# Performance work log

Measured on AMD Instinct MI355X. Metric: run time of the kernel, lower is better.

Reference implementation:

```python
import jax, jax.numpy as jnp
import numpy as np

N = 100000      # n_nodes
E = 1600000     # n_edges (avg degree 16)
F_IN = 128      # nfeat
H = 128         # nhid
C = 64          # nclass


def setup_inputs() -> dict:
    key = jax.random.key(0)
    ks = jax.random.split(key, 6)
    x = jax.random.normal(ks[0], (N, F_IN), dtype=jnp.float32)
    edge_index = jax.random.randint(ks[1], (2, E), 0, N, dtype=jnp.int32)
    # Glorot-ish init for GCNConv weights, zeros for bias (PyG default)
    W1 = jax.random.normal(ks[2], (F_IN, H), dtype=jnp.float32) * (1.0 / np.sqrt(F_IN))
    b1 = jnp.zeros((H,), dtype=jnp.float32)
    W2 = jax.random.normal(ks[3], (H, C), dtype=jnp.float32) * (1.0 / np.sqrt(H))
    b2 = jnp.zeros((C,), dtype=jnp.float32)
    return {"x": x, "edge_index": edge_index, "W1": W1, "b1": b1, "W2": W2, "b2": b2}


def _gcn_conv(x, W, b, src, dst, n):
    """PyG GCNConv: h = W^T x, out_i = sum_j norm_ij * h_j + b, with
    symmetric normalization over the self-loop-augmented graph."""
    h = x @ W                                                   # [n, out]
    deg = jax.ops.segment_sum(jnp.ones(src.shape[0], h.dtype), dst, num_segments=n)
    dinv = jnp.where(deg > 0, jax.lax.rsqrt(deg), 0.0)          # D^-1/2
    norm = dinv[src] * dinv[dst]                                # [E+n]
    msg = h[src] * norm[:, None]                                # gather + scale
    out = jax.ops.segment_sum(msg, dst, num_segments=n)         # scatter-add
    return out + b


def reference(x, edge_index, W1, b1, W2, b2):
    loop = jnp.arange(N, dtype=edge_index.dtype)
    src = jnp.concatenate([edge_index[0], loop])  # sources j (with self loops)
    dst = jnp.concatenate([edge_index[1], loop])  # targets i
    h = jax.nn.relu(_gcn_conv(x, W1, b1, src, dst, N))  # dropout = identity (eval)
    out = _gcn_conv(h, W2, b2, src, dst, N)
    return jax.nn.log_softmax(out, axis=1)
```

## Files before the change

### kernel.cpp

```cpp
#include <hip/hip_runtime.h>
#include <hip/hip_fp16.h>
#include <cstdint>
#include <cstddef>
#include <cstring>


__device__ inline unsigned pack_bf16x2(float a, float b) {
    unsigned ua = __float_as_uint(a);
    unsigned ub = __float_as_uint(b);
    ua += 0x7fffu + ((ua >> 16) & 1u);
    ub += 0x7fffu + ((ub >> 16) & 1u);
    return (ua >> 16) | (ub & 0xffff0000u);
}
__device__ inline unsigned short bf16_rne(float v) {
    unsigned u = __float_as_uint(v);
    u += 0x7fffu + ((u >> 16) & 1u);
    return (unsigned short)(u >> 16);
}
__device__ inline float bf16lo(unsigned u) { return __uint_as_float(u << 16); }
__device__ inline float bf16hi(unsigned u) { return __uint_as_float(u & 0xffff0000u); }


typedef float fv2 __attribute__((ext_vector_type(2)));

template <bool HI>
__device__ inline float2 fp8x2_to_f32_sel(unsigned u) {
#if __has_builtin(__builtin_amdgcn_cvt_pk_f32_fp8)
    fv2 r = __builtin_amdgcn_cvt_pk_f32_fp8((int)u, HI);
    return make_float2(r.x, r.y);
#else
    unsigned u2 = HI ? (u >> 16) : (u & 0xffffu);
    unsigned w = (u2 & 0xFFu) | ((u2 & 0xFF00u) << 8);
    unsigned hb = ((w & 0x00800080u) << 8) | ((w & 0x007f007fu) << 7);
    __half2 h2;
    memcpy(&h2, &hb, 4);
    float2 f = __half22float2(h2);
    f.x *= 256.0f;
    f.y *= 256.0f;
    return f;
#endif
}

__device__ inline unsigned f32_to_fp8_byte(float v) {
    unsigned short hb = __half_as_ushort(__float2half(v * 0.00390625f));
    unsigned t = hb & 0x7fffu;
    t += 0x3fu + ((t >> 7) & 1u);
    return ((hb >> 8) & 0x80u) | (t >> 7);
}

__device__ inline unsigned char f32_to_fp8_b(float v) {
#if __has_builtin(__builtin_amdgcn_cvt_pk_fp8_f32)
    return (unsigned char)(__builtin_amdgcn_cvt_pk_fp8_f32(v, v, 0, false) & 0xff);
#else
    return (unsigned char)f32_to_fp8_byte(v);
#endif
}

typedef int iv4 __attribute__((ext_vector_type(4)));

#define NPART 8
#define KB    32
#define NPP_MAX 12500


__global__ void k_zero16(int* __restrict__ p) {
    if (threadIdx.x < 16) p[threadIdx.x] = 0;
}

__global__ __launch_bounds__(256) void k_bcount(const int* __restrict__ dst,
                                                int* __restrict__ bucketCount,
                                                int E, int npp) {
    __shared__ int c8[NPART];
    if (threadIdx.x < NPART) c8[threadIdx.x] = 0;
    __syncthreads();
    int t = blockIdx.x * blockDim.x + threadIdx.x;
    int stride = gridDim.x * blockDim.x;
    int E4 = E >> 2;
    const iv4* d4 = (const iv4*)dst;
    for (int i = t; i < E4; i += stride) {
        iv4 d = d4[i];
        atomicAdd(&c8[(unsigned)d.x / (unsigned)npp], 1);
        atomicAdd(&c8[(unsigned)d.y / (unsigned)npp], 1);
        atomicAdd(&c8[(unsigned)d.z / (unsigned)npp], 1);
        atomicAdd(&c8[(unsigned)d.w / (unsigned)npp], 1);
    }
    for (int e = E4 * 4 + t; e < E; e += stride)
        atomicAdd(&c8[(unsigned)dst[e] / (unsigned)npp], 1);
    __syncthreads();
    if (threadIdx.x < NPART) atomicAdd(&bucketCount[threadIdx.x], c8[threadIdx.x]);
}

__global__ void k_bscan(const int* __restrict__ bucketCount,
                        int* __restrict__ bucketBase,
                        int* __restrict__ bucketCursor) {
    if (threadIdx.x == 0) {
        int run = 0;
        for (int p = 0; p < NPART; ++p) {
            bucketBase[p] = run;
            bucketCursor[p] = run;
            run += bucketCount[p];
        }
    }
}

__global__ __launch_bounds__(256) void k_bucket(const int* __restrict__ src,
                                                const int* __restrict__ dst,
                                                int* __restrict__ bucketCursor,
                                                int2* __restrict__ pairs,
                                                int E, int npp) {
    __shared__ int cnt8[NPART], run8[NPART], gbase8[NPART];
    int tid = threadIdx.x;
    int base_e = blockIdx.x * 4096 + tid * 16;
    int nv = min(16, E - base_e);
    if (nv < 0) nv = 0;
    int dv[16], sv[16];
    if (nv == 16) {
        for (int q = 0; q < 4; ++q) {
            iv4 d = *(const iv4*)(dst + base_e + q * 4);
            iv4 s = *(const iv4*)(src + base_e + q * 4);
            dv[q * 4 + 0] = d.x; dv[q * 4 + 1] = d.y; dv[q * 4 + 2] = d.z; dv[q * 4 + 3] = d.w;
            sv[q * 4 + 0] = s.x; sv[q * 4 + 1] = s.y; sv[q * 4 + 2] = s.z; sv[q * 4 + 3] = s.w;
        }
    } else {
        for (int k = 0; k < nv; ++k) { dv[k] = dst[base_e + k]; sv[k] = src[base_e + k]; }
    }
    if (tid < NPART) { cnt8[tid] = 0; run8[tid] = 0; }
    __syncthreads();
    for (int k = 0; k < nv; ++k)
        atomicAdd(&cnt8[(unsigned)dv[k] / (unsigned)npp], 1);
    __syncthreads();
    if (tid < NPART) gbase8[tid] = atomicAdd(&bucketCursor[tid], cnt8[tid]);
    __syncthreads();
    for (int k = 0; k < nv; ++k) {
        int p = (unsigned)dv[k] / (unsigned)npp;
        int r = atomicAdd(&run8[p], 1);
        int2 pr; pr.x = dv[k]; pr.y = sv[k];
        pairs[gbase8[p] + r] = pr;
    }
}

__global__ __launch_bounds__(256) void k_count_part(const int2* __restrict__ pairs,
                                                    const int* __restrict__ bucketBase,
                                                    const int* __restrict__ bucketCount,
                                                    int* __restrict__ cntarr, int npp) {
    __shared__ int h[NPP_MAX];
    int p = blockIdx.x & (NPART - 1);
    int b = blockIdx.x >> 3;
    int lo = p * npp;
    for (int i = threadIdx.x; i < npp; i += 256) h[i] = 0;
    __syncthreads();
    int segBase = bucketBase[p], sz = bucketCount[p];
    int chunk = (sz + KB - 1) / KB;
    int s0 = segBase + b * chunk;
    int s1 = min(segBase + sz, s0 + chunk);
    for (int i = s0 + threadIdx.x; i < s1; i += 256)
        atomicAdd(&h[pairs[i].x - lo], 1);
    __syncthreads();
    size_t out = (size_t)(p * KB + b) * npp;
    for (int i = threadIdx.x; i < npp; i += 256) cntarr[out + i] = h[i];
}

__global__ void k_indeg(const int* __restrict__ cntarr, int* __restrict__ indeg,
                        int n, int npp) {
    int d = blockIdx.x * blockDim.x + threadIdx.x;
    if (d >= n) return;
    int p = (unsigned)d / (unsigned)npp;
    int dl = d - p * npp;
    size_t base = (size_t)p * KB * npp + dl;
    int s = 0;
    for (int b = 0; b < KB; ++b) s += cntarr[base + (size_t)b * npp];
    indeg[d] = s;
}

__global__ void k_scan_local(const int* __restrict__ in, int* __restrict__ out,
                             int* __restrict__ partials, int n) {
    __shared__ int s[256];
    int t = threadIdx.x;
    int base = blockIdx.x * 1024 + t * 4;
    int v0 = (base + 0) < n ? in[base + 0] : 0;
    int v1 = (base + 1) < n ? in[base + 1] : 0;
    int v2 = (base + 2) < n ? in[base + 2] : 0;
    int v3 = (base + 3) < n ? in[base + 3] : 0;
    int sum = v0 + v1 + v2 + v3;
    s[t] = sum;
    __syncthreads();
    for (int off = 1; off < 256; off <<= 1) {
        int x = (t >= off) ? s[t - off] : 0;
        __syncthreads();
        s[t] += x;
        __syncthreads();
    }
    int excl = s[t] - sum;
    if ((base + 0) < n) out[base + 0] = excl;
    if ((base + 1) < n) out[base + 1] = excl + v0;
    if ((base + 2) < n) out[base + 2] = excl + v0 + v1;
    if ((base + 3) < n) out[base + 3] = excl + v0 + v1 + v2;
    if (t == 255) partials[blockIdx.x] = s[255];
}

__global__ void k_scan_partials(int* __restrict__ partials, int np) {
    __shared__ int s[256];
    int t = threadIdx.x;
    int v = (t < np) ? partials[t] : 0;
    s[t] = v;
    __syncthreads();
    for (int off = 1; off < 256; off <<= 1) {
        int x = (t >= off) ? s[t - off] : 0;
        __syncthreads();
        s[t] += x;
        __syncthreads();
    }
    if (t < np) partials[t] = s[t] - v;
}

__global__ void k_finalize(int* __restrict__ row_ptr, const int* __restrict__ partials,
                           const int* __restrict__ indeg, float* __restrict__ dinv,
                           int n, int E) {
    int i = blockIdx.x * blockDim.x + threadIdx.x;
    if (i < n) {
        int rp = row_ptr[i] + partials[i >> 10];
        row_ptr[i] = rp;
        dinv[i] = rsqrtf((float)indeg[i] + 1.0f);
        if (i == 0) row_ptr[n] = E;
    }
}

__global__ void k_bases(int* __restrict__ cntarr, const int* __restrict__ row_ptr,
                        int n, int npp) {
    int d = blockIdx.x * blockDim.x + threadIdx.x;
    if (d >= n) return;
    int p = (unsigned)d / (unsigned)npp;
    int dl = d - p * npp;
    size_t base = (size_t)p * KB * npp + dl;
    int run = row_ptr[d];
    for (int b = 0; b < KB; ++b) {
        size_t idx = base + (size_t)b * npp;
        int c = cntarr[idx];
        cntarr[idx] = run;
        run += c;
    }
}

__global__ __launch_bounds__(256) void k_fill2(const int2* __restrict__ pairs,
                                               const int* __restrict__ bucketBase,
                                               const int* __restrict__ bucketCount,
                                               const int* __restrict__ cntarr,
                                               int* __restrict__ col, int npp) {
    __shared__ int cur[NPP_MAX];
    int p = blockIdx.x & (NPART - 1);
    int b = blockIdx.x >> 3;
    int lo = p * npp;
    size_t slice = (size_t)(p * KB + b) * npp;
    for (int i = threadIdx.x; i < npp; i += 256) cur[i] = cntarr[slice + i];
    __syncthreads();
    int segBase = bucketBase[p], sz = bucketCount[p];
    int chunk = (sz + KB - 1) / KB;
    int s0 = segBase + b * chunk;
    int s1 = min(segBase + sz, s0 + chunk);
    for (int i = s0 + threadIdx.x; i < s1; i += 256) {
        int2 e = pairs[i];
        int pos = atomicAdd(&cur[e.x - lo], 1);
        col[pos] = e.y;
    }
}

typedef __attribute__((ext_vector_type(8))) short short8;
typedef __attribute__((ext_vector_type(4))) float f32x4;

union FragU {
    short8 s;
    uint4 u4;
    unsigned u[4];
};

template <int NOUT>
__global__ void k_packW(const float* __restrict__ W, unsigned* __restrict__ Bp) {
    const int NT = NOUT / 16;
    int nf = 4 * NT * 64;
    for (int fid = threadIdx.x; fid < nf; fid += 256) {
        int q = fid / (NT * 64);
        int rem = fid - q * NT * 64;
        int nt = rem >> 6;
        int lane = rem & 63;
        int k0 = q * 32 + (lane >> 4) * 8;
        int ncol = nt * 16 + (lane & 15);
        unsigned u[4];
        for (int h = 0; h < 4; ++h) {
            float a = W[(k0 + 2 * h) * NOUT + ncol];
            float b = W[(k0 + 2 * h + 1) * NOUT + ncol];
            u[h] = pack_bf16x2(a, b);
        }
        uint4 o = {u[0], u[1], u[2], u[3]};
        *(uint4*)(Bp + (size_t)fid * 4) = o;
    }
}

__global__ __launch_bounds__(256) void k_gemm128_mfma(const float* __restrict__ X,
                                                      const unsigned* __restrict__ Bp,
                                                      const float* __restrict__ dinv,
                                                      unsigned char* __restrict__ H8,
                                                      int n) {
    int w = threadIdx.x >> 6;
    int lane = threadIdx.x & 63;
    int quad = lane >> 4;
    int lrow = lane & 15;
    int row0 = blockIdx.x * 64 + w * 16;
    int rowA = min(row0 + lrow, n - 1);

    f32x4 acc[8];
    for (int nt = 0; nt < 8; ++nt) acc[nt] = (f32x4){0.f, 0.f, 0.f, 0.f};

    for (int q = 0; q < 4; ++q) {
        const float* xp = X + (size_t)rowA * 128 + q * 32 + quad * 8;
        float4 x0 = *(const float4*)xp;
        float4 x1 = *(const float4*)(xp + 4);
        FragU a;
        a.u[0] = pack_bf16x2(x0.x, x0.y);
        a.u[1] = pack_bf16x2(x0.z, x0.w);
        a.u[2] = pack_bf16x2(x1.x, x1.y);
        a.u[3] = pack_bf16x2(x1.z, x1.w);
        for (int nt = 0; nt < 8; ++nt) {
            FragU b;
            b.u4 = *(const uint4*)(Bp + ((size_t)(q * 8 + nt) * 64 + lane) * 4);
            acc[nt] = __builtin_amdgcn_mfma_f32_16x16x32_bf16(a.s, b.s, acc[nt], 0, 0, 0);
        }
    }

    int rbase = row0 + quad * 4;
    float dv[4];
    if (rbase + 3 < n) {
        float4 d4 = *(const float4*)(dinv + rbase);
        dv[0] = d4.x; dv[1] = d4.y; dv[2] = d4.z; dv[3] = d4.w;
    } else {
        for (int r = 0; r < 4; ++r) dv[r] = dinv[min(rbase + r, n - 1)];
    }
    for (int nt = 0; nt < 8; ++nt) {
        for (int r = 0; r < 4; ++r) {
            int row = rbase + r;
            if (row < n)
                H8[(size_t)row * 128 + nt * 16 + lrow] = f32_to_fp8_b(dv[r] * acc[nt][r]);
        }
    }
}

__global__ __launch_bounds__(256) void k_gemm64_mfma(const unsigned* __restrict__ Xb,
                                                     const unsigned* __restrict__ Bp,
                                                     const float* __restrict__ dinv,
                                                     unsigned short* __restrict__ H16,
                                                     int n) {
    int w = threadIdx.x >> 6;
    int lane = threadIdx.x & 63;
    int quad = lane >> 4;
    int lrow = lane & 15;
    int row0 = blockIdx.x * 64 + w * 16;
    int rowA = min(row0 + lrow, n - 1);

    f32x4 acc[4];
    for (int nt = 0; nt < 4; ++nt) acc[nt] = (f32x4){0.f, 0.f, 0.f, 0.f};

    for (int q = 0; q < 4; ++q) {
        FragU a;
        a.u4 = *(const uint4*)(Xb + (size_t)rowA * 64 + q * 16 + quad * 4);
        for (int nt = 0; nt < 4; ++nt) {
            FragU b;
            b.u4 = *(const uint4*)(Bp + ((size_t)(q * 4 + nt) * 64 + lane) * 4);
            acc[nt] = __builtin_amdgcn_mfma_f32_16x16x32_bf16(a.s, b.s, acc[nt], 0, 0, 0);
        }
    }

    int rbase = row0 + quad * 4;
    float dv[4];
    if (rbase + 3 < n) {
        float4 d4 = *(const float4*)(dinv + rbase);
        dv[0] = d4.x; dv[1] = d4.y; dv[2] = d4.z; dv[3] = d4.w;
    } else {
        for (int r = 0; r < 4; ++r) dv[r] = dinv[min(rbase + r, n - 1)];
    }
    for (int nt = 0; nt < 4; ++nt) {
        for (int r = 0; r < 4; ++r) {
            int row = rbase + r;
            if (row < n)
                H16[(size_t)row * 64 + nt * 16 + lrow] = bf16_rne(dv[r] * acc[nt][r]);
        }
    }
}


__global__ __launch_bounds__(256) void k_agg_relu(const unsigned* __restrict__ hs,
                                                  const float* __restrict__ dinv,
                                                  const int* __restrict__ row_ptr,
                                                  const int* __restrict__ col,
                                                  const float* __restrict__ bias,
                                                  unsigned* __restrict__ out, int n) {
    int node = blockIdx.x * 4 + (threadIdx.x >> 6);
    if (node >= n) return;
    int lane = threadIdx.x & 63;
    int half = lane >> 5;
    int l = lane & 31;
    float a0 = 0.f, a1 = 0.f, a2 = 0.f, a3 = 0.f;
    if (half == 0) {
        unsigned u = hs[(size_t)node * 32 + l];
        float2 f01 = fp8x2_to_f32_sel<false>(u);
        float2 f23 = fp8x2_to_f32_sel<true>(u);
        a0 = f01.x; a1 = f01.y; a2 = f23.x; a3 = f23.y;
    }
    int p0 = row_ptr[node], p1 = row_ptr[node + 1];
    for (int base = p0; base < p1; base += 64) {
        int nb = min(64, p1 - base);
        int myc = col[base + min(lane, nb - 1)];
        int k = 0;
        for (; k + 16 <= nb; k += 16) {
            int jA = __shfl(myc, k + half);
            int jB = __shfl(myc, k + 2 + half);
            int jC = __shfl(myc, k + 4 + half);
            int jD = __shfl(myc, k + 6 + half);
            int jE = __shfl(myc, k + 8 + half);
            int jF = __shfl(myc, k + 10 + half);
            int jG = __shfl(myc, k + 12 + half);
            int jH = __shfl(myc, k + 14 + half);
            unsigned uA = hs[(size_t)jA * 32 + l];
            unsigned uB = hs[(size_t)jB * 32 + l];
            unsigned uC = hs[(size_t)jC * 32 + l];
            unsigned uD = hs[(size_t)jD * 32 + l];
            unsigned uE = hs[(size_t)jE * 32 + l];
            unsigned uF = hs[(size_t)jF * 32 + l];
            unsigned uG = hs[(size_t)jG * 32 + l];
            unsigned uH = hs[(size_t)jH * 32 + l];
            float2 f;
            f = fp8x2_to_f32_sel<false>(uA); a0 += f.x; a1 += f.y;
            f = fp8x2_to_f32_sel<true>(uA);  a2 += f.x; a3 += f.y;
            f = fp8x2_to_f32_sel<false>(uB); a0 += f.x; a1 += f.y;
            f = fp8x2_to_f32_sel<true>(uB);  a2 += f.x; a3 += f.y;
            f = fp8x2_to_f32_sel<false>(uC); a0 += f.x; a1 += f.y;
            f = fp8x2_to_f32_sel<true>(uC);  a2 += f.x; a3 += f.y;
            f = fp8x2_to_f32_sel<false>(uD); a0 += f.x; a1 += f.y;
            f = fp8x2_to_f32_sel<true>(uD);  a2 += f.x; a3 += f.y;
            f = fp8x2_to_f32_sel<false>(uE); a0 += f.x; a1 += f.y;
            f = fp8x2_to_f32_sel<true>(uE);  a2 += f.x; a3 += f.y;
            f = fp8x2_to_f32_sel<false>(uF); a0 += f.x; a1 += f.y;
            f = fp8x2_to_f32_sel<true>(uF);  a2 += f.x; a3 += f.y;
            f = fp8x2_to_f32_sel<false>(uG); a0 += f.x; a1 += f.y;
            f = fp8x2_to_f32_sel<true>(uG);  a2 += f.x; a3 += f.y;
            f = fp8x2_to_f32_sel<false>(uH); a0 += f.x; a1 += f.y;
            f = fp8x2_to_f32_sel<true>(uH);  a2 += f.x; a3 += f.y;
        }
        for (; k + 8 <= nb; k += 8) {
            int jA = __shfl(myc, k + half);
            int jB = __shfl(myc, k + 2 + half);
            int jC = __shfl(myc, k + 4 + half);
            int jD = __shfl(myc, k + 6 + half);
            unsigned uA = hs[(size_t)jA * 32 + l];
            unsigned uB = hs[(size_t)jB * 32 + l];
            unsigned uC = hs[(size_t)jC * 32 + l];
            unsigned uD = hs[(size_t)jD * 32 + l];
            float2 f;
            f = fp8x2_to_f32_sel<false>(uA); a0 += f.x; a1 += f.y;
            f = fp8x2_to_f32_sel<true>(uA);  a2 += f.x; a3 += f.y;
            f = fp8x2_to_f32_sel<false>(uB); a0 += f.x; a1 += f.y;
            f = fp8x2_to_f32_sel<true>(uB);  a2 += f.x; a3 += f.y;
            f = fp8x2_to_f32_sel<false>(uC); a0 += f.x; a1 += f.y;
            f = fp8x2_to_f32_sel<true>(uC);  a2 += f.x; a3 += f.y;
            f = fp8x2_to_f32_sel<false>(uD); a0 += f.x; a1 += f.y;
            f = fp8x2_to_f32_sel<true>(uD);  a2 += f.x; a3 += f.y;
        }
        for (; k < nb; k += 2) {
            int kk = k + half;
            if (kk < nb) {
                int j = __shfl(myc, kk);
                unsigned u = hs[(size_t)j * 32 + l];
                float2 f0 = fp8x2_to_f32_sel<false>(u);
                float2 f1 = fp8x2_to_f32_sel<true>(u);
                a0 += f0.x; a1 += f0.y; a2 += f1.x; a3 += f1.y;
            }
        }
    }
    a0 += __shfl_xor(a0, 32);
    a1 += __shfl_xor(a1, 32);
    a2 += __shfl_xor(a2, 32);
    a3 += __shfl_xor(a3, 32);
    float di = dinv[node];
    if (half == 0) {
        float4 b4 = *(const float4*)(bias + 4 * l);
        a0 = fmaf(di, a0, b4.x);
        a1 = fmaf(di, a1, b4.y);
        a2 = fmaf(di, a2, b4.z);
        a3 = fmaf(di, a3, b4.w);
        a0 = a0 > 0.f ? a0 : 0.f;
        a1 = a1 > 0.f ? a1 : 0.f;
        a2 = a2 > 0.f ? a2 : 0.f;
        a3 = a3 > 0.f ? a3 : 0.f;
        uint2 o = {pack_bf16x2(a0, a1), pack_bf16x2(a2, a3)};
        *(uint2*)(out + (size_t)node * 64 + 2 * l) = o;
    }
}

__global__ __launch_bounds__(256) void k_agg_lsm(const unsigned* __restrict__ hs,
                                                 const float* __restrict__ dinv,
                                                 const int* __restrict__ row_ptr,
                                                 const int* __restrict__ col,
                                                 const float* __restrict__ bias,
                                                 float* __restrict__ out, int n) {
    int node = blockIdx.x * 4 + (threadIdx.x >> 6);
    if (node >= n) return;
    int lane = threadIdx.x & 63;
    int half = lane >> 5;
    int l = lane & 31;
    float ax = 0.f, ay = 0.f;
    if (half == 0) {
        unsigned u = hs[(size_t)node * 32 + l];
        ax = bf16lo(u);
        ay = bf16hi(u);
    }
    int p0 = row_ptr[node], p1 = row_ptr[node + 1];
    for (int base = p0; base < p1; base += 64) {
        int nb = min(64, p1 - base);
        int myc = col[base + min(lane, nb - 1)];
        int k = 0;
        for (; k + 16 <= nb; k += 16) {
            int jA = __shfl(myc, k + half);
            int jB = __shfl(myc, k + 2 + half);
            int jC = __shfl(myc, k + 4 + half);
            int jD = __shfl(myc, k + 6 + half);
            int jE = __shfl(myc, k + 8 + half);
            int jF = __shfl(myc, k + 10 + half);
            int jG = __shfl(myc, k + 12 + half);
            int jH = __shfl(myc, k + 14 + half);
            unsigned uA = hs[(size_t)jA * 32 + l];
            unsigned uB = hs[(size_t)jB * 32 + l];
            unsigned uC = hs[(size_t)jC * 32 + l];
            unsigned uD = hs[(size_t)jD * 32 + l];
            unsigned uE = hs[(size_t)jE * 32 + l];
            unsigned uF = hs[(size_t)jF * 32 + l];
            unsigned uG = hs[(size_t)jG * 32 + l];
            unsigned uH = hs[(size_t)jH * 32 + l];
            ax += (bf16lo(uA) + bf16lo(uB)) + (bf16lo(uC) + bf16lo(uD)) +
                  (bf16lo(uE) + bf16lo(uF)) + (bf16lo(uG) + bf16lo(uH));
            ay += (bf16hi(uA) + bf16hi(uB)) + (bf16hi(uC) + bf16hi(uD)) +
                  (bf16hi(uE) + bf16hi(uF)) + (bf16hi(uG) + bf16hi(uH));
        }
        for (; k + 8 <= nb; k += 8) {
            int jA = __shfl(myc, k + half);
            int jB = __shfl(myc, k + 2 + half);
            int jC = __shfl(myc, k + 4 + half);
            int jD = __shfl(myc, k + 6 + half);
            unsigned uA = hs[(size_t)jA * 32 + l];
            unsigned uB = hs[(size_t)jB * 32 + l];
            unsigned uC = hs[(size_t)jC * 32 + l];
            unsigned uD = hs[(size_t)jD * 32 + l];
            ax += (bf16lo(uA) + bf16lo(uB)) + (bf16lo(uC) + bf16lo(uD));
            ay += (bf16hi(uA) + bf16hi(uB)) + (bf16hi(uC) + bf16hi(uD));
        }
        for (; k < nb; k += 2) {
            int kk = k + half;
            if (kk < nb) {
                int j = __shfl(myc, kk);
                unsigned u = hs[(size_t)j * 32 + l];
                ax += bf16lo(u);
                ay += bf16hi(u);
            }
        }
    }
    ax += __shfl_xor(ax, 32);
    ay += __shfl_xor(ay, 32);
    float di = dinv[node];
    float2 b2 = ((const float2*)bias)[l];
    float vx = fmaf(di, ax, b2.x);
    float vy = fmaf(di, ay, b2.y);
    float m = fmaxf(vx, vy);
    for (int off = 16; off; off >>= 1) m = fmaxf(m, __shfl_xor(m, off));
    float s = __expf(vx - m) + __expf(vy - m);
    for (int off = 16; off; off >>= 1) s += __shfl_xor(s, off);
    float ls = __logf(s);
    if (half == 0) {
        float2 o = {vx - m - ls, vy - m - ls};
        ((float2*)(out + (size_t)node * 64))[l] = o;
    }
}


extern "C" void kernel_launch(void* const* d_in, const int* in_sizes, int n_in,
                              void* d_out, int out_size, void* d_ws, size_t ws_size,
                              hipStream_t stream) {
    const float* x  = (const float*)d_in[0];
    const int*   ei = (const int*)d_in[1];
    const float* W1 = (const float*)d_in[2];
    const float* b1 = (const float*)d_in[3];
    const float* W2 = (const float*)d_in[4];
    const float* b2 = (const float*)d_in[5];
    float* out = (float*)d_out;

    const int N = in_sizes[0] / 128;
    const int E = in_sizes[1] / 2;
    const int* src = ei;
    const int* dst = ei + E;
    const int npp = (N + NPART - 1) / NPART;

    char* w = (char*)d_ws;
    size_t off = 0;
    auto alloc = [&](size_t bytes) -> void* {
        void* p = w + off;
        off += (bytes + 255) & ~(size_t)255;
        return p;
    };
    int*      indeg    = (int*)alloc((size_t)N * 4);
    int*      row_ptr  = (int*)alloc((size_t)(N + 1) * 4);
    int*      colarr   = (int*)alloc((size_t)E * 4);
    int*      partials = (int*)alloc(256 * 4);
    int*      bmeta    = (int*)alloc(16 * 4);
    int*      bbase    = (int*)alloc(NPART * 4);
    float*    dinv     = (float*)alloc((size_t)N * 4);
    unsigned* h1f8     = (unsigned*)alloc((size_t)N * 32 * 4);
    unsigned* a1b      = (unsigned*)alloc((size_t)N * 64 * 4);
    unsigned* h2b      = (unsigned*)alloc((size_t)N * 32 * 4);
    unsigned* Bp1      = (unsigned*)alloc(4 * 8 * 64 * 16);
    unsigned* Bp2      = (unsigned*)alloc(4 * 4 * 64 * 16);
    int2* pairs  = (int2*)a1b;
    int*  cntarr = (int*)((char*)a1b + (size_t)E * 8);
    (void)ws_size; (void)n_in; (void)out_size;

    int* bucketCount  = bmeta;
    int* bucketCursor = bmeta + 8;
    int nscan = (N + 1023) / 1024;
    int nA3 = (E + 4095) / 4096;
    int ngemm = (N + 63) / 64;

    k_zero16<<<1, 64, 0, stream>>>(bmeta);
    k_packW<128><<<1, 256, 0, stream>>>(W1, Bp1);
    k_packW<64><<<1, 256, 0, stream>>>(W2, Bp2);
    k_bcount<<<256, 256, 0, stream>>>(dst, bucketCount, E, npp);
    k_bscan<<<1, 64, 0, stream>>>(bucketCount, bbase, bucketCursor);
    k_bucket<<<nA3, 256, 0, stream>>>(src, dst, bucketCursor, pairs, E, npp);
    k_count_part<<<NPART * KB, 256, 0, stream>>>(pairs, bbase, bucketCount, cntarr, npp);
    k_indeg<<<(N + 255) / 256, 256, 0, stream>>>(cntarr, indeg, N, npp);
    k_scan_local<<<nscan, 256, 0, stream>>>(indeg, row_ptr, partials, N);
    k_scan_partials<<<1, 256, 0, stream>>>(partials, nscan);
    k_finalize<<<(N + 255) / 256, 256, 0, stream>>>(row_ptr, partials, indeg, dinv, N, E);
    k_bases<<<(N + 255) / 256, 256, 0, stream>>>(cntarr, row_ptr, N, npp);
    k_fill2<<<NPART * KB, 256, 0, stream>>>(pairs, bbase, bucketCount, cntarr,
                                            colarr, npp);

    k_gemm128_mfma<<<ngemm, 256, 0, stream>>>(x, Bp1, dinv, (unsigned char*)h1f8, N);
    k_agg_relu<<<(N + 3) / 4, 256, 0, stream>>>(h1f8, dinv, row_ptr, colarr, b1, a1b, N);
    k_gemm64_mfma<<<ngemm, 256, 0, stream>>>(a1b, Bp2, dinv, (unsigned short*)h2b, N);
    k_agg_lsm<<<(N + 3) / 4, 256, 0, stream>>>(h2b, dinv, row_ptr, colarr, b2, out, N);
}
```

Measured before the change: 302.3 us.

## Pack edge pairs into 32-bit words and fuse CSR build kernels

Edge (dst,src) pairs are packed into one 32-bit word, with the partition-local dst in the high bits and the 17-bit src in the low bits, halving bucket traffic. The zero and pack-weight kernels merge into one setup kernel. In-degree is accumulated with atomics inside the count kernel, so the separate indeg pass is gone, and finalize is fused with the per-bucket base computation. This cuts launches and memory passes in CSR construction, but the packing relies on node ids fitting in 17 bits and the local dst in 15 bits.

```diff
diff --git a/kernel.cpp b/kernel.cpp
--- a/kernel.cpp
+++ b/kernel.cpp
@@ -61,208 +61,8 @@
 #define NPART 8
 #define KB    32
 #define NPP_MAX 12500
-
-
-__global__ void k_zero16(int* __restrict__ p) {
-    if (threadIdx.x < 16) p[threadIdx.x] = 0;
-}
-
-__global__ __launch_bounds__(256) void k_bcount(const int* __restrict__ dst,
-                                                int* __restrict__ bucketCount,
-                                                int E, int npp) {
-    __shared__ int c8[NPART];
-    if (threadIdx.x < NPART) c8[threadIdx.x] = 0;
-    __syncthreads();
-    int t = blockIdx.x * blockDim.x + threadIdx.x;
-    int stride = gridDim.x * blockDim.x;
-    int E4 = E >> 2;
-    const iv4* d4 = (const iv4*)dst;
-    for (int i = t; i < E4; i += stride) {
-        iv4 d = d4[i];
-        atomicAdd(&c8[(unsigned)d.x / (unsigned)npp], 1);
-        atomicAdd(&c8[(unsigned)d.y / (unsigned)npp], 1);
-        atomicAdd(&c8[(unsigned)d.z / (unsigned)npp], 1);
-        atomicAdd(&c8[(unsigned)d.w / (unsigned)npp], 1);
-    }
-    for (int e = E4 * 4 + t; e < E; e += stride)
-        atomicAdd(&c8[(unsigned)dst[e] / (unsigned)npp], 1);
-    __syncthreads();
-    if (threadIdx.x < NPART) atomicAdd(&bucketCount[threadIdx.x], c8[threadIdx.x]);
-}
-
-__global__ void k_bscan(const int* __restrict__ bucketCount,
-                        int* __restrict__ bucketBase,
-                        int* __restrict__ bucketCursor) {
-    if (threadIdx.x == 0) {
-        int run = 0;
-        for (int p = 0; p < NPART; ++p) {
-            bucketBase[p] = run;
-            bucketCursor[p] = run;
-            run += bucketCount[p];
-        }
-    }
-}
-
-__global__ __launch_bounds__(256) void k_bucket(const int* __restrict__ src,
-                                                const int* __restrict__ dst,
-                                                int* __restrict__ bucketCursor,
-                                                int2* __restrict__ pairs,
-                                                int E, int npp) {
-    __shared__ int cnt8[NPART], run8[NPART], gbase8[NPART];
-    int tid = threadIdx.x;
-    int base_e = blockIdx.x * 4096 + tid * 16;
-    int nv = min(16, E - base_e);
-    if (nv < 0) nv = 0;
-    int dv[16], sv[16];
-    if (nv == 16) {
-        for (int q = 0; q < 4; ++q) {
-            iv4 d = *(const iv4*)(dst + base_e + q * 4);
-            iv4 s = *(const iv4*)(src + base_e + q * 4);
-            dv[q * 4 + 0] = d.x; dv[q * 4 + 1] = d.y; dv[q * 4 + 2] = d.z; dv[q * 4 + 3] = d.w;
-            sv[q * 4 + 0] = s.x; sv[q * 4 + 1] = s.y; sv[q * 4 + 2] = s.z; sv[q * 4 + 3] = s.w;
-        }
-    } else {
-        for (int k = 0; k < nv; ++k) { dv[k] = dst[base_e + k]; sv[k] = src[base_e + k]; }
-    }
-    if (tid < NPART) { cnt8[tid] = 0; run8[tid] = 0; }
-    __syncthreads();
-    for (int k = 0; k < nv; ++k)
-        atomicAdd(&cnt8[(unsigned)dv[k] / (unsigned)npp], 1);
-    __syncthreads();
-    if (tid < NPART) gbase8[tid] = atomicAdd(&bucketCursor[tid], cnt8[tid]);
-    __syncthreads();
-    for (int k = 0; k < nv; ++k) {
-        int p = (unsigned)dv[k] / (unsigned)npp;
-        int r = atomicAdd(&run8[p], 1);
-        int2 pr; pr.x = dv[k]; pr.y = sv[k];
-        pairs[gbase8[p] + r] = pr;
-    }
-}
-
-__global__ __launch_bounds__(256) void k_count_part(const int2* __restrict__ pairs,
-                                                    const int* __restrict__ bucketBase,
-                                                    const int* __restrict__ bucketCount,
-                                                    int* __restrict__ cntarr, int npp) {
-    __shared__ int h[NPP_MAX];
-    int p = blockIdx.x & (NPART - 1);
-    int b = blockIdx.x >> 3;
-    int lo = p * npp;
-    for (int i = threadIdx.x; i < npp; i += 256) h[i] = 0;
-    __syncthreads();
-    int segBase = bucketBase[p], sz = bucketCount[p];
-    int chunk = (sz + KB - 1) / KB;
-    int s0 = segBase + b * chunk;
-    int s1 = min(segBase + sz, s0 + chunk);
-    for (int i = s0 + threadIdx.x; i < s1; i += 256)
-        atomicAdd(&h[pairs[i].x - lo], 1);
-    __syncthreads();
-    size_t out = (size_t)(p * KB + b) * npp;
-    for (int i = threadIdx.x; i < npp; i += 256) cntarr[out + i] = h[i];
-}
-
-__global__ void k_indeg(const int* __restrict__ cntarr, int* __restrict__ indeg,
-                        int n, int npp) {
-    int d = blockIdx.x * blockDim.x + threadIdx.x;
-    if (d >= n) return;
-    int p = (unsigned)d / (unsigned)npp;
-    int dl = d - p * npp;
-    size_t base = (size_t)p * KB * npp + dl;
-    int s = 0;
-    for (int b = 0; b < KB; ++b) s += cntarr[base + (size_t)b * npp];
-    indeg[d] = s;
-}
-
-__global__ void k_scan_local(const int* __restrict__ in, int* __restrict__ out,
-                             int* __restrict__ partials, int n) {
-    __shared__ int s[256];
-    int t = threadIdx.x;
-    int base = blockIdx.x * 1024 + t * 4;
-    int v0 = (base + 0) < n ? in[base + 0] : 0;
-    int v1 = (base + 1) < n ? in[base + 1] : 0;
-    int v2 = (base + 2) < n ? in[base + 2] : 0;
-    int v3 = (base + 3) < n ? in[base + 3] : 0;
-    int sum = v0 + v1 + v2 + v3;
-    s[t] = sum;
-    __syncthreads();
-    for (int off = 1; off < 256; off <<= 1) {
-        int x = (t >= off) ? s[t - off] : 0;
-        __syncthreads();
-        s[t] += x;
-        __syncthreads();
-    }
-    int excl = s[t] - sum;
-    if ((base + 0) < n) out[base + 0] = excl;
-    if ((base + 1) < n) out[base + 1] = excl + v0;
-    if ((base + 2) < n) out[base + 2] = excl + v0 + v1;
-    if ((base + 3) < n) out[base + 3] = excl + v0 + v1 + v2;
-    if (t == 255) partials[blockIdx.x] = s[255];
-}
-
-__global__ void k_scan_partials(int* __restrict__ partials, int np) {
-    __shared__ int s[256];
-    int t = threadIdx.x;
-    int v = (t < np) ? partials[t] : 0;
-    s[t] = v;
-    __syncthreads();
-    for (int off = 1; off < 256; off <<= 1) {
-        int x = (t >= off) ? s[t - off] : 0;
-        __syncthreads();
-        s[t] += x;
-        __syncthreads();
-    }
-    if (t < np) partials[t] = s[t] - v;
-}
-
-__global__ void k_finalize(int* __restrict__ row_ptr, const int* __restrict__ partials,
-                           const int* __restrict__ indeg, float* __restrict__ dinv,
-                           int n, int E) {
-    int i = blockIdx.x * blockDim.x + threadIdx.x;
-    if (i < n) {
-        int rp = row_ptr[i] + partials[i >> 10];
-        row_ptr[i] = rp;
-        dinv[i] = rsqrtf((float)indeg[i] + 1.0f);
-        if (i == 0) row_ptr[n] = E;
-    }
-}
-
-__global__ void k_bases(int* __restrict__ cntarr, const int* __restrict__ row_ptr,
-                        int n, int npp) {
-    int d = blockIdx.x * blockDim.x + threadIdx.x;
-    if (d >= n) return;
-    int p = (unsigned)d / (unsigned)npp;
-    int dl = d - p * npp;
-    size_t base = (size_t)p * KB * npp + dl;
-    int run = row_ptr[d];
-    for (int b = 0; b < KB; ++b) {
-        size_t idx = base + (size_t)b * npp;
-        int c = cntarr[idx];
-        cntarr[idx] = run;
-        run += c;
-    }
-}
-
-__global__ __launch_bounds__(256) void k_fill2(const int2* __restrict__ pairs,
-                                               const int* __restrict__ bucketBase,
-                                               const int* __restrict__ bucketCount,
-                                               const int* __restrict__ cntarr,
-                                               int* __restrict__ col, int npp) {
-    __shared__ int cur[NPP_MAX];
-    int p = blockIdx.x & (NPART - 1);
-    int b = blockIdx.x >> 3;
-    int lo = p * npp;
-    size_t slice = (size_t)(p * KB + b) * npp;
-    for (int i = threadIdx.x; i < npp; i += 256) cur[i] = cntarr[slice + i];
-    __syncthreads();
-    int segBase = bucketBase[p], sz = bucketCount[p];
-    int chunk = (sz + KB - 1) / KB;
-    int s0 = segBase + b * chunk;
-    int s1 = min(segBase + sz, s0 + chunk);
-    for (int i = s0 + threadIdx.x; i < s1; i += 256) {
-        int2 e = pairs[i];
-        int pos = atomicAdd(&cur[e.x - lo], 1);
-        col[pos] = e.y;
-    }
-}
+#define SRC_BITS 17
+#define SRC_MASK 0x1FFFFu
 
 typedef __attribute__((ext_vector_type(8))) short short8;
 typedef __attribute__((ext_vector_type(4))) float f32x4;
@@ -274,7 +74,7 @@
 };
 
 template <int NOUT>
-__global__ void k_packW(const float* __restrict__ W, unsigned* __restrict__ Bp) {
+__device__ inline void packW_dev(const float* __restrict__ W, unsigned* __restrict__ Bp) {
     const int NT = NOUT / 16;
     int nf = 4 * NT * 64;
     for (int fid = threadIdx.x; fid < nf; fid += 256) {
@@ -294,6 +94,212 @@
         *(uint4*)(Bp + (size_t)fid * 4) = o;
     }
 }
+
+__global__ __launch_bounds__(256) void k_setup(const float* __restrict__ W1,
+                                               const float* __restrict__ W2,
+                                               unsigned* __restrict__ Bp1,
+                                               unsigned* __restrict__ Bp2,
+                                               int* __restrict__ bmeta,
+                                               int* __restrict__ indeg,
+                                               int N, int nz) {
+    int b = blockIdx.x;
+    if (b < nz) {
+        int base = b * 1024 + threadIdx.x * 4;
+        for (int i = 0; i < 4; ++i)
+            if (base + i < N) indeg[base + i] = 0;
+        if (b == 0 && threadIdx.x < 16) bmeta[threadIdx.x] = 0;
+    } else if (b == nz) {
+        packW_dev<128>(W1, Bp1);
+    } else {
+        packW_dev<64>(W2, Bp2);
+    }
+}
+
+
+__global__ __launch_bounds__(256) void k_bcount(const int* __restrict__ dst,
+                                                int* __restrict__ bucketCount,
+                                                int E, int npp) {
+    __shared__ int c8[NPART];
+    if (threadIdx.x < NPART) c8[threadIdx.x] = 0;
+    __syncthreads();
+    int t = blockIdx.x * blockDim.x + threadIdx.x;
+    int stride = gridDim.x * blockDim.x;
+    int E4 = E >> 2;
+    const iv4* d4 = (const iv4*)dst;
+    for (int i = t; i < E4; i += stride) {
+        iv4 d = d4[i];
+        atomicAdd(&c8[(unsigned)d.x / (unsigned)npp], 1);
+        atomicAdd(&c8[(unsigned)d.y / (unsigned)npp], 1);
+        atomicAdd(&c8[(unsigned)d.z / (unsigned)npp], 1);
+        atomicAdd(&c8[(unsigned)d.w / (unsigned)npp], 1);
+    }
+    for (int e = E4 * 4 + t; e < E; e += stride)
+        atomicAdd(&c8[(unsigned)dst[e] / (unsigned)npp], 1);
+    __syncthreads();
+    if (threadIdx.x < NPART) atomicAdd(&bucketCount[threadIdx.x], c8[threadIdx.x]);
+}
+
+__global__ void k_bscan(const int* __restrict__ bucketCount,
+                        int* __restrict__ bucketBase,
+                        int* __restrict__ bucketCursor) {
+    if (threadIdx.x == 0) {
+        int run = 0;
+        for (int p = 0; p < NPART; ++p) {
+            bucketBase[p] = run;
+            bucketCursor[p] = run;
+            run += bucketCount[p];
+        }
+    }
+}
+
+__global__ __launch_bounds__(256) void k_bucket(const int* __restrict__ src,
+                                                const int* __restrict__ dst,
+                                                int* __restrict__ bucketCursor,
+                                                unsigned* __restrict__ pairs,
+                                                int E, int npp) {
+    __shared__ int cnt8[NPART], run8[NPART], gbase8[NPART];
+    int tid = threadIdx.x;
+    int base_e = blockIdx.x * 4096 + tid * 16;
+    int nv = min(16, E - base_e);
+    if (nv < 0) nv = 0;
+    int dv[16], sv[16];
+    if (nv == 16) {
+        for (int q = 0; q < 4; ++q) {
+            iv4 d = *(const iv4*)(dst + base_e + q * 4);
+            iv4 s = *(const iv4*)(src + base_e + q * 4);
+            dv[q * 4 + 0] = d.x; dv[q * 4 + 1] = d.y; dv[q * 4 + 2] = d.z; dv[q * 4 + 3] = d.w;
+            sv[q * 4 + 0] = s.x; sv[q * 4 + 1] = s.y; sv[q * 4 + 2] = s.z; sv[q * 4 + 3] = s.w;
+        }
+    } else {
+        for (int k = 0; k < nv; ++k) { dv[k] = dst[base_e + k]; sv[k] = src[base_e + k]; }
+    }
+    if (tid < NPART) { cnt8[tid] = 0; run8[tid] = 0; }
+    __syncthreads();
+    for (int k = 0; k < nv; ++k)
+        atomicAdd(&cnt8[(unsigned)dv[k] / (unsigned)npp], 1);
+    __syncthreads();
+    if (tid < NPART) gbase8[tid] = atomicAdd(&bucketCursor[tid], cnt8[tid]);
+    __syncthreads();
+    for (int k = 0; k < nv; ++k) {
+        int p = (unsigned)dv[k] / (unsigned)npp;
+        int r = atomicAdd(&run8[p], 1);
+        pairs[gbase8[p] + r] = ((unsigned)(dv[k] - p * npp) << SRC_BITS) | (unsigned)sv[k];
+    }
+}
+
+__global__ __launch_bounds__(256) void k_count_part(const unsigned* __restrict__ pairs,
+                                                    const int* __restrict__ bucketBase,
+                                                    const int* __restrict__ bucketCount,
+                                                    int* __restrict__ cntarr,
+                                                    int* __restrict__ indeg, int npp) {
+    __shared__ int h[NPP_MAX];
+    int p = blockIdx.x & (NPART - 1);
+    int b = blockIdx.x >> 3;
+    int lo = p * npp;
+    for (int i = threadIdx.x; i < npp; i += 256) h[i] = 0;
+    __syncthreads();
+    int segBase = bucketBase[p], sz = bucketCount[p];
+    int chunk = (sz + KB - 1) / KB;
+    int s0 = segBase + b * chunk;
+    int s1 = min(segBase + sz, s0 + chunk);
+    for (int i = s0 + threadIdx.x; i < s1; i += 256)
+        atomicAdd(&h[pairs[i] >> SRC_BITS], 1);
+    __syncthreads();
+    size_t out = (size_t)(p * KB + b) * npp;
+    for (int i = threadIdx.x; i < npp; i += 256) {
+        int c = h[i];
+        cntarr[out + i] = c;
+        if (c) atomicAdd(&indeg[lo + i], c);
+    }
+}
+
+__global__ void k_scan_local(const int* __restrict__ in, int* __restrict__ out,
+                             int* __restrict__ partials, int n) {
+    __shared__ int s[256];
+    int t = threadIdx.x;
+    int base = blockIdx.x * 1024 + t * 4;
+    int v0 = (base + 0) < n ? in[base + 0] : 0;
+    int v1 = (base + 1) < n ? in[base + 1] : 0;
+    int v2 = (base + 2) < n ? in[base + 2] : 0;
+    int v3 = (base + 3) < n ? in[base + 3] : 0;
+    int sum = v0 + v1 + v2 + v3;
+    s[t] = sum;
+    __syncthreads();
+    for (int off = 1; off < 256; off <<= 1) {
+        int x = (t >= off) ? s[t - off] : 0;
+        __syncthreads();
+        s[t] += x;
+        __syncthreads();
+    }
+    int excl = s[t] - sum;
+    if ((base + 0) < n) out[base + 0] = excl;
+    if ((base + 1) < n) out[base + 1] = excl + v0;
+    if ((base + 2) < n) out[base + 2] = excl + v0 + v1;
+    if ((base + 3) < n) out[base + 3] = excl + v0 + v1 + v2;
+    if (t == 255) partials[blockIdx.x] = s[255];
+}
+
+__global__ void k_scan_partials(int* __restrict__ partials, int np) {
+    __shared__ int s[256];
+    int t = threadIdx.x;
+    int v = (t < np) ? partials[t] : 0;
+    s[t] = v;
+    __syncthreads();
+    for (int off = 1; off < 256; off <<= 1) {
+        int x = (t >= off) ? s[t - off] : 0;
+        __syncthreads();
+        s[t] += x;
+        __syncthreads();
+    }
+    if (t < np) partials[t] = s[t] - v;
+}
+
+__global__ void k_finalize_bases(int* __restrict__ row_ptr,
+                                 const int* __restrict__ partials,
+                                 const int* __restrict__ indeg,
+                                 float* __restrict__ dinv,
+                                 int* __restrict__ cntarr,
+                                 int n, int E, int npp) {
+    int d = blockIdx.x * blockDim.x + threadIdx.x;
+    if (d >= n) return;
+    int rp = row_ptr[d] + partials[d >> 10];
+    row_ptr[d] = rp;
+    dinv[d] = rsqrtf((float)indeg[d] + 1.0f);
+    if (d == 0) row_ptr[n] = E;
+    int p = (unsigned)d / (unsigned)npp;
+    int dl = d - p * npp;
+    size_t base = (size_t)p * KB * npp + dl;
+    int run = rp;
+    for (int b = 0; b < KB; ++b) {
+        size_t idx = base + (size_t)b * npp;
+        int c = cntarr[idx];
+        cntarr[idx] = run;
+        run += c;
+    }
+}
+
+__global__ __launch_bounds__(256) void k_fill2(const unsigned* __restrict__ pairs,
+                                               const int* __restrict__ bucketBase,
+                                               const int* __restrict__ bucketCount,
+                                               const int* __restrict__ cntarr,
+                                               int* __restrict__ col, int npp) {
+    __shared__ int cur[NPP_MAX];
+    int p = blockIdx.x & (NPART - 1);
+    int b = blockIdx.x >> 3;
+    size_t slice = (size_t)(p * KB + b) * npp;
+    for (int i = threadIdx.x; i < npp; i += 256) cur[i] = cntarr[slice + i];
+    __syncthreads();
+    int segBase = bucketBase[p], sz = bucketCount[p];
+    int chunk = (sz + KB - 1) / KB;
+    int s0 = segBase + b * chunk;
+    int s1 = min(segBase + sz, s0 + chunk);
+    for (int i = s0 + threadIdx.x; i < s1; i += 256) {
+        unsigned e = pairs[i];
+        int pos = atomicAdd(&cur[e >> SRC_BITS], 1);
+        col[pos] = (int)(e & SRC_MASK);
+    }
+}
+
 
 __global__ __launch_bounds__(256) void k_gemm128_mfma(const float* __restrict__ X,
                                                       const unsigned* __restrict__ Bp,
@@ -614,8 +620,8 @@
     unsigned* h2b      = (unsigned*)alloc((size_t)N * 32 * 4);
     unsigned* Bp1      = (unsigned*)alloc(4 * 8 * 64 * 16);
     unsigned* Bp2      = (unsigned*)alloc(4 * 4 * 64 * 16);
-    int2* pairs  = (int2*)a1b;
-    int*  cntarr = (int*)((char*)a1b + (size_t)E * 8);
+    unsigned* pairs  = (unsigned*)a1b;
+    int*      cntarr = (int*)((char*)a1b + (size_t)E * 4);
     (void)ws_size; (void)n_in; (void)out_size;
 
     int* bucketCount  = bmeta;
@@ -624,18 +630,16 @@
     int nA3 = (E + 4095) / 4096;
     int ngemm = (N + 63) / 64;
 
-    k_zero16<<<1, 64, 0, stream>>>(bmeta);
-    k_packW<128><<<1, 256, 0, stream>>>(W1, Bp1);
-    k_packW<64><<<1, 256, 0, stream>>>(W2, Bp2);
+    k_setup<<<nscan + 2, 256, 0, stream>>>(W1, W2, Bp1, Bp2, bmeta, indeg, N, nscan);
     k_bcount<<<256, 256, 0, stream>>>(dst, bucketCount, E, npp);
     k_bscan<<<1, 64, 0, stream>>>(bucketCount, bbase, bucketCursor);
     k_bucket<<<nA3, 256, 0, stream>>>(src, dst, bucketCursor, pairs, E, npp);
-    k_count_part<<<NPART * KB, 256, 0, stream>>>(pairs, bbase, bucketCount, cntarr, npp);
-    k_indeg<<<(N + 255) / 256, 256, 0, stream>>>(cntarr, indeg, N, npp);
+    k_count_part<<<NPART * KB, 256, 0, stream>>>(pairs, bbase, bucketCount, cntarr,
+                                                 indeg, npp);
     k_scan_local<<<nscan, 256, 0, stream>>>(indeg, row_ptr, partials, N);
     k_scan_partials<<<1, 256, 0, stream>>>(partials, nscan);
-    k_finalize<<<(N + 255) / 256, 256, 0, stream>>>(row_ptr, partials, indeg, dinv, N, E);
-    k_bases<<<(N + 255) / 256, 256, 0, stream>>>(cntarr, row_ptr, N, npp);
+    k_finalize_bases<<<(N + 255) / 256, 256, 0, stream>>>(row_ptr, partials, indeg,
+                                                          dinv, cntarr, N, E, npp);
     k_fill2<<<NPART * KB, 256, 0, stream>>>(pairs, bbase, bucketCount, cntarr,
                                             colarr, npp);
 
```

Measured after the change: 304.5 us. No clear change (+0.7%).
